# Kernel tuning notes

Measured on AMD Instinct MI355X. Metric: run time of the kernel, lower is better.

The kernel has to match this reference:

```python
import jax, jax.numpy as jnp
import numpy as np

B, S, D, K, DF, H, DFF = 2, 512, 512, 8, 64, 8, 2048
DH = D // H  # d_head = 64
CS = D // K  # chunk_size = 64


def layer_norm(x, g, b, eps=1e-5):
    m = x.mean(-1, keepdims=True)
    v = ((x - m) ** 2).mean(-1, keepdims=True)
    return (x - m) / jnp.sqrt(v + eps) * g + b


def matexp_taylor(M, terms=6):
    # exp(M) ~= I + M + M^2/2! + ... (6 terms), batched over leading dims
    I = jnp.broadcast_to(jnp.eye(M.shape[-1], dtype=M.dtype), M.shape)
    res, P = I, I
    for n in range(1, terms + 1):
        P = jnp.matmul(P, M) / n
        res = res + P
    return res


def setup_inputs() -> dict:
    key = jax.random.key(0)
    ks = jax.random.split(key, 24)
    w = lambda k, shape, s=0.02: (jax.random.normal(k, shape, jnp.float32) * s)
    return {
        'x': jax.random.normal(ks[0], (B, S, D), jnp.float32),
        'u': jax.random.normal(ks[1], (B, S, DF), jnp.float32),
        'Wq': w(ks[2], (D, D)), 'bq': jnp.zeros((D,), jnp.float32),
        'Wk': w(ks[3], (D, D)), 'bk': jnp.zeros((D,), jnp.float32),
        'Wv': w(ks[4], (D, D)), 'bv': jnp.zeros((D,), jnp.float32),
        'Wo': w(ks[5], (D, D)), 'bo': jnp.zeros((D,), jnp.float32),
        'Wfp': w(ks[6], (DF, D)), 'bfp': jnp.zeros((D,), jnp.float32),
        'Wfo': w(ks[7], (D, DF)), 'bfo': jnp.zeros((DF,), jnp.float32),
        'Wc1': w(ks[8], (D, DFF)), 'bc1': jnp.zeros((DFF,), jnp.float32),
        'g_ln': jnp.ones((DFF,), jnp.float32), 'b_ln': jnp.zeros((DFF,), jnp.float32),
        # small scale keeps the Lie elements O(1) so the Taylor matexp is well-behaved
        'Wc2': w(ks[9], (DFF, D * K * K), 0.001), 'bc2': jnp.zeros((D * K * K,), jnp.float32),
    }


def reference(x, u, Wq, bq, Wk, bk, Wv, bv, Wo, bo, Wfp, bfp, Wfo, bfo,
              Wc1, bc1, g_ln, b_ln, Wc2, bc2):
    b, s, d = x.shape
    # --- ConnectionNetwork: A[b,s,d,k,k] ---
    h = jax.nn.gelu(x @ Wc1 + bc1, approximate=False)
    h = layer_norm(h, g_ln, b_ln)
    A = (h @ Wc2 + bc2).reshape(b, s, d, K, K)
    # --- ParallelTransport: lie[b,i,j] = sum_d (x_i - x_j)_d * A[j,d]  ---
    # (split into x_i.A_j and x_j.A_j terms to avoid [b,s,s,d,k,k] intermediate)
    lie = jnp.einsum('bid,bjdkl->bijkl', x, A) - jnp.einsum('bjd,bjdkl->bjkl', x, A)[:, None]
    Gamma = matexp_taylor(-lie)  # [b,s,s,k,k], Gamma[b,i,j] transports j->i
    # --- standard multi-head attention on x (eval mode, no dropout, no mask) ---
    q = (x @ Wq + bq).reshape(b, s, H, DH).transpose(0, 2, 1, 3)
    k_ = (x @ Wk + bk).reshape(b, s, H, DH).transpose(0, 2, 1, 3)
    v = (x @ Wv + bv).reshape(b, s, H, DH).transpose(0, 2, 1, 3)
    scores = jnp.einsum('bhid,bhjd->bhij', q, k_) / jnp.sqrt(jnp.float32(DH))
    attn = jax.nn.softmax(scores, axis=-1)
    ctx = jnp.einsum('bhij,bhjd->bhid', attn, v).transpose(0, 2, 1, 3).reshape(b, s, d)
    x_out = x + ctx @ Wo + bo
    # --- fiber transport: u_i += sum_j attn_avg[i,j] * Gamma[i,j] @ u_chunks[j] ---
    u_proj = u @ Wfp + bfp                      # [b,s,D]
    u_chunks = u_proj.reshape(b, s, K, CS)      # [b,s,k,cs]
    attn_avg = attn.mean(axis=1)                # [b,s,s]
    weighted = Gamma * attn_avg[..., None, None]
    u_t = jnp.einsum('bijkl,bjlc->bikc', weighted, u_chunks).reshape(b, s, d)
    u_out = u + u_t @ Wfo + bfo
    return (x_out, u_out)
```

## Files before the change

kernel.cpp:

```cpp
#include <hip/hip_runtime.h>
#include <math.h>

#define BB 2
#define SS 512
#define DD 512
#define HH 8
#define DFF 2048

typedef __attribute__((ext_vector_type(8))) short bf16x8;
typedef __attribute__((ext_vector_type(4))) float f32x4;

__device__ __forceinline__ float gelu_exact(float v) {
    return 0.5f * v * (1.0f + erff(v * 0.70710678118654752f));
}
__device__ __forceinline__ unsigned short f2bf(float f) {
    unsigned u = __float_as_uint(f);
    u += 0x7FFF + ((u >> 16) & 1);
    return (unsigned short)(u >> 16);
}
__device__ __forceinline__ float bf2f(unsigned short s) {
    return __uint_as_float(((unsigned)s) << 16);
}
__device__ __forceinline__ void gload16(const void* g, void* l) {
    __builtin_amdgcn_global_load_lds((const __attribute__((address_space(1))) void*)g,
                                     (__attribute__((address_space(3))) void*)l, 16, 0, 0);
}

template<int NT, int EPI>
__global__ __launch_bounds__(256)
void mgemm_k(const unsigned short* __restrict__ A, const unsigned short* __restrict__ B,
             const float* __restrict__ bias, const float* __restrict__ resid,
             float* __restrict__ Cf, unsigned short* __restrict__ Cb,
             int K, int lda, int ldb, int ldc, int batchH,
             long aSB, long aSH, long bSB, long bSH, long cSB, long cSH,
             float scale)
{
    __shared__ unsigned short As[128][32];
    __shared__ unsigned short Bs[NT][32];
    const int tid = threadIdx.x;
    const int wave = tid >> 6, lane = tid & 63;
    const int z = blockIdx.z;
    const int zb = z / batchH, zh = z % batchH;
    const unsigned short* Ab = A + (long)zb * aSB + (long)zh * aSH;
    const unsigned short* Bb = B + (long)zb * bSB + (long)zh * bSH;
    const int row0 = blockIdx.y * 128, col0 = blockIdx.x * NT;
    const int wm = wave >> 1, wn = wave & 1;
    const int lm = lane & 15, quad = lane >> 4;
    const int lrow = lane >> 2, lk = (lane & 3) * 8;
    constexpr int NTW = NT / 32;
    f32x4 acc[4][NTW];
    #pragma unroll
    for (int i = 0; i < 4; ++i)
        #pragma unroll
        for (int j = 0; j < NTW; ++j) acc[i][j] = (f32x4)0.f;

    for (int k0 = 0; k0 < K; k0 += 32) {
        #pragma unroll
        for (int t = 0; t < 2; ++t) {
            const int r = wave * 32 + t * 16;
            gload16(Ab + (long)(row0 + r + lrow) * lda + k0 + lk, &As[r][0]);
        }
        if (NT == 128) {
            #pragma unroll
            for (int t = 0; t < 2; ++t) {
                const int r = wave * 32 + t * 16;
                gload16(Bb + (long)(col0 + r + lrow) * ldb + k0 + lk, &Bs[r][0]);
            }
        } else {
            const int r = wave * 16;
            gload16(Bb + (long)(col0 + r + lrow) * ldb + k0 + lk, &Bs[r][0]);
        }
        __syncthreads();
        bf16x8 af[4], bfr[NTW];
        #pragma unroll
        for (int mt = 0; mt < 4; ++mt)
            af[mt] = *(const bf16x8*)&As[wm * 64 + mt * 16 + lm][quad * 8];
        #pragma unroll
        for (int nt = 0; nt < NTW; ++nt)
            bfr[nt] = *(const bf16x8*)&Bs[wn * (NT / 2) + nt * 16 + lm][quad * 8];
        #pragma unroll
        for (int mt = 0; mt < 4; ++mt)
            #pragma unroll
            for (int nt = 0; nt < NTW; ++nt)
                acc[mt][nt] = __builtin_amdgcn_mfma_f32_16x16x32_bf16(
                    af[mt], bfr[nt], acc[mt][nt], 0, 0, 0);
        __syncthreads();
    }
    float* Cfz = Cf ? Cf + (long)zb * cSB + (long)zh * cSH : nullptr;
    unsigned short* Cbz = Cb ? Cb + (long)zb * cSB + (long)zh * cSH : nullptr;
    #pragma unroll
    for (int mt = 0; mt < 4; ++mt) {
        #pragma unroll
        for (int nt = 0; nt < NTW; ++nt) {
            #pragma unroll
            for (int r = 0; r < 4; ++r) {
                const int row = row0 + wm * 64 + mt * 16 + quad * 4 + r;
                const int col = col0 + wn * (NT / 2) + nt * 16 + lm;
                float v = acc[mt][nt][r] * scale;
                if (EPI == 2)      v += bias[(col & 511) * 64 + (col >> 9)];
                else if (EPI == 1 || EPI == 4) v += bias[col];
                else if ((EPI == 3 || EPI == 5 || EPI == 6) && bias) v += bias[col];
                if (EPI == 1) v = gelu_exact(v);
                if (EPI == 4) v += resid[(long)row * ldc + col];
                if (EPI == 0 || EPI == 1 || EPI == 4)
                    Cfz[(long)row * ldc + col] = v;
                else if (EPI == 2 || EPI == 3)
                    Cbz[(long)row * ldc + col] = f2bf(v);
                else if (EPI == 5)
                    Cb[(long)(row >> 9) * 262144 + (col >> 6) * 32768 +
                       (col & 63) * 512 + (row & 511)] = f2bf(v);
                else if (EPI == 6)
                    Cb[(long)(row >> 9) * 262144 + (col & 63) * 4096 +
                       (row & 511) * 8 + (col >> 6)] = f2bf(v);
            }
        }
    }
}

__global__ __launch_bounds__(512, 2)
void fc2_k(const unsigned short* __restrict__ A, const unsigned short* __restrict__ Bm,
           const float* __restrict__ bias, unsigned short* __restrict__ C)
{
    extern __shared__ unsigned short smraw[];
#define SMA(ab, h) (smraw + (((ab) * 2 + (h)) * 8192))
#define SMB(bb, h) (smraw + (32768 + ((bb) * 2 + (h)) * 8192))
    const int tid = threadIdx.x;
    const int wave = tid >> 6, lane = tid & 63;
    const int bid = blockIdx.x;
    const int lin = (bid & 7) * 64 + (bid >> 3);
    const int by = lin & 3, bx = lin >> 2;
    const int row0 = by * 256, col0 = bx * 256;
    const int wm = wave >> 2, wn = wave & 3;
    const int lm = lane & 15, quad = lane >> 4;
    const int axor = lm & 7;
    const int arow = (wm * 64 + lm) * 64;
    const int brow = (wn * 32 + lm) * 64;
    const int ca0 = ((quad) ^ axor) * 8;
    const int ca1 = ((quad + 4) ^ axor) * 8;
    const int srow = wave * 8 + (lane >> 3);
    const int scx = ((lane & 7) ^ ((lane >> 3) & 7)) * 8;
    const int sbrow = ((srow >> 5) << 6) + (srow & 31);
    const unsigned short* AgB = A + (long)(row0 + srow) * 2048 + scx;
    const unsigned short* BgB = Bm + (long)(col0 + sbrow) * 2048 + scx;

    f32x4 acc[8][4];
    #pragma unroll
    for (int i = 0; i < 8; ++i)
        #pragma unroll
        for (int j = 0; j < 4; ++j) acc[i][j] = (f32x4)0.f;
    bf16x8 afr[4][2], b0f[2][2], b1f[2][2];

#define STGA(ab, h, toff) do { \
        const unsigned short* _g = AgB + (toff) * 64 + (h) * (64 * 2048); \
        unsigned short* _d = SMA(ab, h) + wave * 512; \
        gload16(_g, _d); \
        gload16(_g + 128 * 2048, _d + 4096); \
    } while (0)
#define STGB(bb, h, toff) do { \
        const unsigned short* _g = BgB + (toff) * 64 + (h) * (32 * 2048); \
        unsigned short* _d = SMB(bb, h) + wave * 512; \
        gload16(_g, _d); \
        gload16(_g + 128 * 2048, _d + 4096); \
    } while (0)
#define RDA(Hp) do { _Pragma("unroll") for (int _m = 0; _m < 4; ++_m) { \
        afr[_m][0] = *(const bf16x8*)((Hp) + arow + _m * 1024 + ca0); \
        afr[_m][1] = *(const bf16x8*)((Hp) + arow + _m * 1024 + ca1); } } while (0)
#define RDB(bf, Hp) do { _Pragma("unroll") for (int _n = 0; _n < 2; ++_n) { \
        bf[_n][0] = *(const bf16x8*)((Hp) + brow + _n * 1024 + ca0); \
        bf[_n][1] = *(const bf16x8*)((Hp) + brow + _n * 1024 + ca1); } } while (0)
#define MM(QM, QN, bf) do { _Pragma("unroll") for (int _m = 0; _m < 4; ++_m) \
        _Pragma("unroll") for (int _n = 0; _n < 2; ++_n) { \
        acc[(QM)*4+_m][(QN)*2+_n] = __builtin_amdgcn_mfma_f32_16x16x32_bf16( \
            afr[_m][0], bf[_n][0], acc[(QM)*4+_m][(QN)*2+_n], 0, 0, 0); \
        acc[(QM)*4+_m][(QN)*2+_n] = __builtin_amdgcn_mfma_f32_16x16x32_bf16( \
            afr[_m][1], bf[_n][1], acc[(QM)*4+_m][(QN)*2+_n], 0, 0, 0); } } while (0)
#define PH_MID() \
        __builtin_amdgcn_s_barrier(); \
        asm volatile("s_waitcnt lgkmcnt(0)" ::: "memory"); \
        __builtin_amdgcn_sched_barrier(0); \
        __builtin_amdgcn_s_setprio(1)
#define PH_END(VM) \
        __builtin_amdgcn_s_setprio(0); \
        __builtin_amdgcn_sched_barrier(0); \
        asm volatile("s_waitcnt vmcnt(" #VM ")" ::: "memory"); \
        __builtin_amdgcn_sched_barrier(0); \
        __builtin_amdgcn_s_barrier()
#define PH_END_NW() \
        __builtin_amdgcn_s_setprio(0); \
        __builtin_amdgcn_sched_barrier(0); \
        __builtin_amdgcn_s_barrier()

    STGB(0, 0, 0);
    STGB(0, 1, 0);
    STGA(0, 0, 0);
    STGA(0, 1, 0);
    STGB(1, 0, 1);
    STGB(1, 1, 1);
    asm volatile("s_waitcnt vmcnt(6)" ::: "memory");
    __builtin_amdgcn_s_barrier();

    int rA = 0;
    int rB = 0, mB = 1, wB = 2;
    #pragma unroll 1
    for (int t = 0; t < 32; ++t) {
        const int tA = (t + 1 < 32) ? (t + 1) : 31;
        const int tB = (t + 2 < 32) ? (t + 2) : 31;
        const unsigned short* A0p = SMA(rA, 0);
        const unsigned short* A1p = SMA(rA, 1);
        const unsigned short* B0p = SMB(rB, 0);
        const unsigned short* B1p = SMB(rB, 1);
        RDA(A0p); RDB(b0f, B0p);
        STGA(rA ^ 1, 0, tA);
        PH_MID(); MM(0, 0, b0f); PH_END_NW();
        RDB(b1f, B1p);
        STGA(rA ^ 1, 1, tA);
        PH_MID(); MM(0, 1, b1f); PH_END(8);
        RDA(A1p);
        STGB(wB, 0, tB);
        PH_MID(); MM(1, 1, b1f); PH_END_NW();
        STGB(wB, 1, tB);
        PH_MID(); MM(1, 0, b0f); PH_END(6);
        rA ^= 1;
        const int tmp = rB; rB = mB; mB = wB; wB = tmp;
    }
    asm volatile("s_waitcnt vmcnt(0)" ::: "memory");

    const int crow = row0 + wm * 128 + quad * 4;
    const int ccol0 = col0 + wn * 64 + lm;
    #pragma unroll
    for (int ms = 0; ms < 8; ++ms)
        #pragma unroll
        for (int ns = 0; ns < 4; ++ns) {
            const int col = ccol0 + ns * 16;
            const float bv = bias[(col & 511) * 64 + (col >> 9)];
            #pragma unroll
            for (int r = 0; r < 4; ++r) {
                const int row = crow + ms * 16 + r;
                C[(long)row * 32768 + col] = f2bf(acc[ms][ns][r] + bv);
            }
        }
#undef SMA
#undef SMB
#undef STGA
#undef STGB
#undef RDA
#undef RDB
#undef MM
#undef PH_MID
#undef PH_END
#undef PH_END_NW
}

__global__ __launch_bounds__(256)
void liegamma_k(const unsigned short* __restrict__ xb, const unsigned short* __restrict__ At,
                const float* __restrict__ xa, const float* __restrict__ aavg,
                unsigned short* __restrict__ Gw)
{
    __shared__ unsigned short Xs[128][32];
    __shared__ unsigned short Ts[64][32];
    __shared__ float Ml[128][68];
    const int tid = threadIdx.x;
    const int wave = tid >> 6, lane = tid & 63;
    const int b = blockIdx.z, j = blockIdx.y;
    const int i0 = blockIdx.x * 128;
    const int lm = lane & 15, quad = lane >> 4;
    const int lrow = lane >> 2, lk = (lane & 3) * 8;
    const unsigned short* Xb = xb + ((long)b * 512 + i0) * 512;
    const unsigned short* Tb = At + ((long)(b * 512 + j)) * 32768;
    f32x4 acc[2][4];
    #pragma unroll
    for (int i = 0; i < 2; ++i)
        #pragma unroll
        for (int n = 0; n < 4; ++n) acc[i][n] = (f32x4)0.f;

    for (int k0 = 0; k0 < 512; k0 += 32) {
        #pragma unroll
        for (int t = 0; t < 2; ++t) {
            const int r = wave * 32 + t * 16;
            gload16(Xb + (long)(r + lrow) * 512 + k0 + lk, &Xs[r][0]);
        }
        {
            const int r = wave * 16;
            gload16(Tb + (long)(r + lrow) * 512 + k0 + lk, &Ts[r][0]);
        }
        __syncthreads();
        bf16x8 af[2], bfr[4];
        #pragma unroll
        for (int mt = 0; mt < 2; ++mt)
            af[mt] = *(const bf16x8*)&Xs[wave * 32 + mt * 16 + lm][quad * 8];
        #pragma unroll
        for (int nt = 0; nt < 4; ++nt)
            bfr[nt] = *(const bf16x8*)&Ts[nt * 16 + lm][quad * 8];
        #pragma unroll
        for (int mt = 0; mt < 2; ++mt)
            #pragma unroll
            for (int nt = 0; nt < 4; ++nt)
                acc[mt][nt] = __builtin_amdgcn_mfma_f32_16x16x32_bf16(
                    af[mt], bfr[nt], acc[mt][nt], 0, 0, 0);
        __syncthreads();
    }
    const float* xar = xa + ((long)(b * 512 + j)) * 64;
    #pragma unroll
    for (int mt = 0; mt < 2; ++mt)
        #pragma unroll
        for (int nt = 0; nt < 4; ++nt) {
            const float xv = xar[nt * 16 + lm];
            #pragma unroll
            for (int r = 0; r < 4; ++r)
                Ml[wave * 32 + mt * 16 + quad * 4 + r][nt * 16 + lm] = xv - acc[mt][nt][r];
        }
    __syncthreads();
    const int r8 = tid & 7, mg = tid >> 3;
    #pragma unroll 1
    for (int pass = 0; pass < 4; ++pass) {
        const int mi = pass * 32 + mg;
        const f32x4* Mr = (const f32x4*)&Ml[mi][0];
        f32x4 Mreg[16];
        #pragma unroll
        for (int l = 0; l < 16; ++l) Mreg[l] = Mr[l];
        float P[8], res[8];
        #pragma unroll
        for (int c = 0; c < 8; ++c) { const float iv = (c == r8) ? 1.f : 0.f; P[c] = iv; res[c] = iv; }
        #pragma unroll
        for (int n = 1; n <= 6; ++n) {
            float tmp[8] = {0.f,0.f,0.f,0.f,0.f,0.f,0.f,0.f};
            const float invn = 1.f / (float)n;
            #pragma unroll
            for (int l = 0; l < 8; ++l) {
                const f32x4 m0 = Mreg[l * 2], m1 = Mreg[l * 2 + 1];
                const float pl = P[l];
                #pragma unroll
                for (int c = 0; c < 4; ++c) {
                    tmp[c]     = fmaf(pl, m0[c], tmp[c]);
                    tmp[4 + c] = fmaf(pl, m1[c], tmp[4 + c]);
                }
            }
            #pragma unroll
            for (int c = 0; c < 8; ++c) { P[c] = tmp[c] * invn; res[c] += P[c]; }
        }
        const float av = aavg[((long)b * 512 + i0 + mi) * 512 + j];
        bf16x8 o;
        #pragma unroll
        for (int c = 0; c < 8; ++c) o[c] = (short)f2bf(res[c] * av);
        *(bf16x8*)(Gw + ((long)(b * 8 + r8) * 512 + (i0 + mi)) * 4096 + (long)j * 8) = o;
    }
}

__global__ __launch_bounds__(256)
void lnbf_k(const float* __restrict__ h, const float* __restrict__ g,
            const float* __restrict__ b, unsigned short* __restrict__ out)
{
    const long row = blockIdx.x;
    const float* r = h + row * (long)DFF;
    const int tid = threadIdx.x;
    float vals[8];
    float s = 0.f, sq = 0.f;
    #pragma unroll
    for (int e = 0; e < 8; ++e) {
        const float v = r[tid + e * 256];
        vals[e] = v; s += v; sq += v * v;
    }
    __shared__ float rs[256], rq[256];
    rs[tid] = s; rq[tid] = sq; __syncthreads();
    for (int st = 128; st > 0; st >>= 1) {
        if (tid < st) { rs[tid] += rs[tid + st]; rq[tid] += rq[tid + st]; }
        __syncthreads();
    }
    const float mean = rs[0] * (1.f / DFF);
    const float var  = rq[0] * (1.f / DFF) - mean * mean;
    const float inv  = rsqrtf(var + 1e-5f);
    unsigned short* o = out + row * (long)DFF;
    #pragma unroll
    for (int e = 0; e < 8; ++e) {
        const int c = tid + e * 256;
        o[c] = f2bf((vals[e] - mean) * inv * g[c] + b[c]);
    }
}

__global__ __launch_bounds__(256)
void xa_k(const float* __restrict__ x, const unsigned short* __restrict__ At,
          float* __restrict__ xa)
{
    const int bj = blockIdx.x;
    const int tid = threadIdx.x;
    const int kl = tid >> 2, q = tid & 3;
    const unsigned short* Ar = At + (long)bj * 32768 + kl * 512 + q * 128;
    const float* xr = x + (long)bj * 512 + q * 128;
    float s = 0.f;
    #pragma unroll
    for (int d0 = 0; d0 < 128; d0 += 8) {
        const bf16x8 a = *(const bf16x8*)&Ar[d0];
        const f32x4 x0 = *(const f32x4*)&xr[d0];
        const f32x4 x1 = *(const f32x4*)&xr[d0 + 4];
        s = fmaf(x0[0], bf2f((unsigned short)a[0]), s);
        s = fmaf(x0[1], bf2f((unsigned short)a[1]), s);
        s = fmaf(x0[2], bf2f((unsigned short)a[2]), s);
        s = fmaf(x0[3], bf2f((unsigned short)a[3]), s);
        s = fmaf(x1[0], bf2f((unsigned short)a[4]), s);
        s = fmaf(x1[1], bf2f((unsigned short)a[5]), s);
        s = fmaf(x1[2], bf2f((unsigned short)a[6]), s);
        s = fmaf(x1[3], bf2f((unsigned short)a[7]), s);
    }
    __shared__ float red[64][5];
    red[kl][q] = s; __syncthreads();
    if (q == 0)
        xa[(long)bj * 64 + kl] = red[kl][0] + red[kl][1] + red[kl][2] + red[kl][3];
}

__global__ __launch_bounds__(256)
void softmax_k(float* __restrict__ p, unsigned short* __restrict__ pb)
{
    const long row = blockIdx.x;
    float* r = p + row * 512;
    const int tid = threadIdx.x;
    float v0 = r[tid], v1 = r[tid + 256];
    __shared__ float red[256];
    red[tid] = fmaxf(v0, v1); __syncthreads();
    for (int s = 128; s > 0; s >>= 1) {
        if (tid < s) red[tid] = fmaxf(red[tid], red[tid + s]);
        __syncthreads();
    }
    const float m = red[0]; __syncthreads();
    v0 = expf(v0 - m); v1 = expf(v1 - m);
    red[tid] = v0 + v1; __syncthreads();
    for (int s = 128; s > 0; s >>= 1) {
        if (tid < s) red[tid] += red[tid + s];
        __syncthreads();
    }
    const float inv = 1.f / red[0];
    const float a0 = v0 * inv, a1 = v1 * inv;
    r[tid] = a0; r[tid + 256] = a1;
    unsigned short* rb = pb + row * 512;
    rb[tid] = f2bf(a0); rb[tid + 256] = f2bf(a1);
}

__global__ __launch_bounds__(256)
void aavg_k(const float* __restrict__ attn, float* __restrict__ aavg)
{
    const long idx = (long)blockIdx.x * 256 + threadIdx.x;
    const int b = (int)(idx >> 18);
    const long rem = idx & 262143;
    float s = 0.f;
    #pragma unroll
    for (int h = 0; h < HH; ++h)
        s += attn[(long)b * 2097152 + (long)h * 262144 + rem];
    aavg[idx] = s * 0.125f;
}

__global__ __launch_bounds__(256)
void tconv_k(const float* __restrict__ in, unsigned short* __restrict__ out,
             int R, int C)
{
    __shared__ float Ls[64][65];
    const int c0 = blockIdx.x * 64, r0 = blockIdx.y * 64;
    const int tid = threadIdx.x;
    const int tc = tid & 63, tr = tid >> 6;
    #pragma unroll
    for (int p = 0; p < 16; ++p)
        Ls[tr + p * 4][tc] = in[(long)(r0 + tr + p * 4) * C + c0 + tc];
    __syncthreads();
    #pragma unroll
    for (int p = 0; p < 16; ++p)
        out[(long)(c0 + tr + p * 4) * R + r0 + tc] = f2bf(Ls[tc][tr + p * 4]);
}

__global__ __launch_bounds__(256)
void wc2p_k(const float* __restrict__ in, unsigned short* __restrict__ out)
{
    __shared__ float Ls[64][65];
    const int d0 = blockIdx.x;
    const long f0 = blockIdx.y * 64;
    const int tid = threadIdx.x;
    const int tc = tid & 63, tr = tid >> 6;
    #pragma unroll
    for (int p = 0; p < 16; ++p)
        Ls[tr + p * 4][tc] = in[(f0 + tr + p * 4) * 32768 + (long)d0 * 64 + tc];
    __syncthreads();
    #pragma unroll
    for (int p = 0; p < 16; ++p) {
        const int kl = tr + p * 4;
        out[((long)kl * 512 + d0) * 2048 + f0 + tc] = f2bf(Ls[tc][kl]);
    }
}

__global__ __launch_bounds__(256)
void f2bf_k(const float* __restrict__ in, unsigned short* __restrict__ out, int n)
{
    const int i = blockIdx.x * 256 + threadIdx.x;
    if (i < n) out[i] = f2bf(in[i]);
}

extern "C" void kernel_launch(void* const* d_in, const int* in_sizes, int n_in,
                              void* d_out, int out_size, void* d_ws, size_t ws_size,
                              hipStream_t stream) {
    const float* x   = (const float*)d_in[0];
    const float* u   = (const float*)d_in[1];
    const float* Wq  = (const float*)d_in[2];  const float* bq  = (const float*)d_in[3];
    const float* Wk  = (const float*)d_in[4];  const float* bk  = (const float*)d_in[5];
    const float* Wv  = (const float*)d_in[6];  const float* bv  = (const float*)d_in[7];
    const float* Wo  = (const float*)d_in[8];  const float* bo  = (const float*)d_in[9];
    const float* Wfp = (const float*)d_in[10]; const float* bfp = (const float*)d_in[11];
    const float* Wfo = (const float*)d_in[12]; const float* bfo = (const float*)d_in[13];
    const float* Wc1 = (const float*)d_in[14]; const float* bc1 = (const float*)d_in[15];
    const float* gln = (const float*)d_in[16]; const float* bln = (const float*)d_in[17];
    const float* Wc2 = (const float*)d_in[18]; const float* bc2 = (const float*)d_in[19];

    float* ws = (float*)d_ws;
    unsigned short* Wc2p = (unsigned short*)(ws);
    unsigned short* Gw   = (unsigned short*)(ws);
    unsigned short* At   = (unsigned short*)(ws + 33554432);
    float*          h    = ws + 50331648;
    unsigned short* h_bf = (unsigned short*)(ws + 52428800);
    unsigned short* x_bf = (unsigned short*)(ws + 53477376);
    unsigned short* u_bf = (unsigned short*)(ws + 53739520);
    unsigned short* Wc1t = (unsigned short*)(ws + 53772288);
    unsigned short* Wqt  = (unsigned short*)(ws + 54296576);
    unsigned short* Wkt  = (unsigned short*)(ws + 54427648);
    unsigned short* Wvt  = (unsigned short*)(ws + 54558720);
    unsigned short* Wot  = (unsigned short*)(ws + 54689792);
    unsigned short* Wfpt = (unsigned short*)(ws + 54820864);
    unsigned short* Wfot = (unsigned short*)(ws + 54837248);
    float*          xa   = ws + 54853632;
    unsigned short* q_bf = (unsigned short*)(ws + 54919168);
    unsigned short* k_bf = (unsigned short*)(ws + 55181312);
    unsigned short* vT   = (unsigned short*)(ws + 55443456);
    float*          sc   = ws + 55705600;
    unsigned short* at_bf= (unsigned short*)(ws + 59899904);
    float*          av   = ws + 61997056;
    unsigned short* ctx  = (unsigned short*)(ws + 62521344);
    unsigned short* upT2 = (unsigned short*)(ws + 62783488);
    unsigned short* ut_bf= (unsigned short*)(ws + 63045632);
    float* xout = (float*)d_out;
    float* uout = xout + 524288;

    const dim3 blk(256);

    hipFuncSetAttribute(reinterpret_cast<const void*>(fc2_k),
                        hipFuncAttributeMaxDynamicSharedMemorySize, 163840);

    tconv_k<<<dim3(32, 8), blk, 0, stream>>>(Wc1, Wc1t, 512, 2048);
    tconv_k<<<dim3(8, 8), blk, 0, stream>>>(Wq, Wqt, 512, 512);
    tconv_k<<<dim3(8, 8), blk, 0, stream>>>(Wk, Wkt, 512, 512);
    tconv_k<<<dim3(8, 8), blk, 0, stream>>>(Wv, Wvt, 512, 512);
    tconv_k<<<dim3(8, 8), blk, 0, stream>>>(Wo, Wot, 512, 512);
    tconv_k<<<dim3(8, 1), blk, 0, stream>>>(Wfp, Wfpt, 64, 512);
    tconv_k<<<dim3(1, 8), blk, 0, stream>>>(Wfo, Wfot, 512, 64);
    wc2p_k<<<dim3(512, 32), blk, 0, stream>>>(Wc2, Wc2p);
    f2bf_k<<<dim3(2048), blk, 0, stream>>>(x, x_bf, 524288);
    f2bf_k<<<dim3(256), blk, 0, stream>>>(u, u_bf, 65536);

    mgemm_k<128,3><<<dim3(4, 8, 1), blk, 0, stream>>>(
        x_bf, Wqt, bq, nullptr, nullptr, q_bf, 512, 512, 512, 512,
        1, 0,0,0,0,0,0, 1.0f);
    mgemm_k<128,3><<<dim3(4, 8, 1), blk, 0, stream>>>(
        x_bf, Wkt, bk, nullptr, nullptr, k_bf, 512, 512, 512, 512,
        1, 0,0,0,0,0,0, 1.0f);
    mgemm_k<128,5><<<dim3(4, 8, 1), blk, 0, stream>>>(
        x_bf, Wvt, bv, nullptr, nullptr, vT, 512, 512, 512, 512,
        1, 0,0,0,0,0,0, 1.0f);
    mgemm_k<128,0><<<dim3(4, 4, 16), blk, 0, stream>>>(
        q_bf, k_bf, nullptr, nullptr, sc, nullptr, 64, 512, 512, 512,
        8, 262144,64, 262144,64, 2097152,262144, 0.125f);
    softmax_k<<<dim3(BB * HH * SS), blk, 0, stream>>>(sc, at_bf);
    aavg_k<<<dim3(2048), blk, 0, stream>>>(sc, av);
    mgemm_k<64,3><<<dim3(1, 4, 16), blk, 0, stream>>>(
        at_bf, vT, nullptr, nullptr, nullptr, ctx, 512, 512, 512, 512,
        8, 2097152,262144, 262144,32768, 262144,64, 1.0f);
    mgemm_k<128,4><<<dim3(4, 8, 1), blk, 0, stream>>>(
        ctx, Wot, bo, x, xout, nullptr, 512, 512, 512, 512,
        1, 0,0,0,0,0,0, 1.0f);

    mgemm_k<128,1><<<dim3(16, 8, 1), blk, 0, stream>>>(
        x_bf, Wc1t, bc1, nullptr, h, nullptr, 512, 512, 512, 2048,
        1, 0,0,0,0,0,0, 1.0f);
    lnbf_k<<<dim3(1024), blk, 0, stream>>>(h, gln, bln, h_bf);
    fc2_k<<<dim3(512), dim3(512), 163840, stream>>>(h_bf, Wc2p, bc2, At);
    xa_k<<<dim3(1024), blk, 0, stream>>>(x, At, xa);
    liegamma_k<<<dim3(4, 512, 2), blk, 0, stream>>>(x_bf, At, xa, av, Gw);

    mgemm_k<128,6><<<dim3(4, 8, 1), blk, 0, stream>>>(
        u_bf, Wfpt, bfp, nullptr, nullptr, upT2, 64, 64, 64, 512,
        1, 0,0,0,0,0,0, 1.0f);
    mgemm_k<64,3><<<dim3(1, 4, 16), blk, 0, stream>>>(
        Gw, upT2, nullptr, nullptr, nullptr, ut_bf, 4096, 4096, 4096, 512,
        8, 16777216,2097152, 262144,0, 262144,64, 1.0f);
    mgemm_k<64,4><<<dim3(1, 8, 1), blk, 0, stream>>>(
        ut_bf, Wfot, bfo, u, uout, nullptr, 512, 512, 512, 64,
        1, 0,0,0,0,0,0, 1.0f);
}
```

Before: 944.1 us.

## Split-K the small GEMMs with separate fp32 partial-sum reduction kernels

Adds a split-K template parameter to the MFMA GEMM so each block covers only a slice of the K dimension and writes fp32 partials. The Q/K/V projections, attn@V, the Wo projection, the Gamma-weighted transport GEMM and the Wfo projection now launch 4-8x more blocks. Small reduction kernels then sum the partials and apply bias, residual and layout transforms. This targets low occupancy on a large-CU GPU, since those GEMMs previously launched only 16-64 blocks. The cost is extra kernel launches and extra global traffic for the fp32 partials.

Result: faster. 866.1 us (-8.3%).

```diff
diff --git a/kernel.cpp b/kernel.cpp
--- a/kernel.cpp
+++ b/kernel.cpp
@@ -26,7 +26,7 @@
                                      (__attribute__((address_space(3))) void*)l, 16, 0, 0);
 }
 
-template<int NT, int EPI>
+template<int NT, int EPI, int SK = 1>
 __global__ __launch_bounds__(256)
 void mgemm_k(const unsigned short* __restrict__ A, const unsigned short* __restrict__ B,
              const float* __restrict__ bias, const float* __restrict__ resid,
@@ -43,7 +43,9 @@
     const int zb = z / batchH, zh = z % batchH;
     const unsigned short* Ab = A + (long)zb * aSB + (long)zh * aSH;
     const unsigned short* Bb = B + (long)zb * bSB + (long)zh * bSH;
-    const int row0 = blockIdx.y * 128, col0 = blockIdx.x * NT;
+    const int chunk = (SK > 1) ? ((int)blockIdx.x % SK) : 0;
+    const int colb  = (SK > 1) ? ((int)blockIdx.x / SK) : (int)blockIdx.x;
+    const int row0 = blockIdx.y * 128, col0 = colb * NT;
     const int wm = wave >> 1, wn = wave & 1;
     const int lm = lane & 15, quad = lane >> 4;
     const int lrow = lane >> 2, lk = (lane & 3) * 8;
@@ -54,7 +56,8 @@
         #pragma unroll
         for (int j = 0; j < NTW; ++j) acc[i][j] = (f32x4)0.f;
 
-    for (int k0 = 0; k0 < K; k0 += 32) {
+    const int kLo = chunk * (K / SK), kHi = kLo + K / SK;
+    for (int k0 = kLo; k0 < kHi; k0 += 32) {
         #pragma unroll
         for (int t = 0; t < 2; ++t) {
             const int r = wave * 32 + t * 16;
@@ -86,7 +89,7 @@
                     af[mt], bfr[nt], acc[mt][nt], 0, 0, 0);
         __syncthreads();
     }
-    float* Cfz = Cf ? Cf + (long)zb * cSB + (long)zh * cSH : nullptr;
+    float* Cfz = (Cf && EPI != 7) ? Cf + (long)zb * cSB + (long)zh * cSH : Cf;
     unsigned short* Cbz = Cb ? Cb + (long)zb * cSB + (long)zh * cSH : nullptr;
     #pragma unroll
     for (int mt = 0; mt < 4; ++mt) {
@@ -104,6 +107,8 @@
                 if (EPI == 4) v += resid[(long)row * ldc + col];
                 if (EPI == 0 || EPI == 1 || EPI == 4)
                     Cfz[(long)row * ldc + col] = v;
+                else if (EPI == 7)
+                    Cf[(long)z * cSB + (long)chunk * cSH + (long)row * ldc + col] = v;
                 else if (EPI == 2 || EPI == 3)
                     Cbz[(long)row * ldc + col] = f2bf(v);
                 else if (EPI == 5)
@@ -115,6 +120,56 @@
             }
         }
     }
+}
+
+__global__ __launch_bounds__(256)
+void redqk_k(const float* __restrict__ p, const float* __restrict__ bias,
+             unsigned short* __restrict__ out)
+{
+    const long idx = (long)blockIdx.x * 256 + threadIdx.x;
+    const float s = p[idx] + p[idx + 524288] + p[idx + 1048576] + p[idx + 1572864]
+                  + bias[idx & 511];
+    out[idx] = f2bf(s);
+}
+__global__ __launch_bounds__(256)
+void redv_k(const float* __restrict__ p, const float* __restrict__ bias,
+            unsigned short* __restrict__ vT)
+{
+    const long idx = (long)blockIdx.x * 256 + threadIdx.x;
+    const int col = (int)(idx & 511);
+    const float s = p[idx] + p[idx + 524288] + p[idx + 1048576] + p[idx + 1572864]
+                  + bias[col];
+    vT[(idx >> 18) * 262144 + (col >> 6) * 32768 + (col & 63) * 512 +
+       ((idx >> 9) & 511)] = f2bf(s);
+}
+__global__ __launch_bounds__(256)
+void redwo_k(const float* __restrict__ p, const float* __restrict__ bias,
+             const float* __restrict__ resid, float* __restrict__ out)
+{
+    const long idx = (long)blockIdx.x * 256 + threadIdx.x;
+    out[idx] = resid[idx] + bias[idx & 511]
+             + p[idx] + p[idx + 524288] + p[idx + 1048576] + p[idx + 1572864];
+}
+template<int SK>
+__global__ __launch_bounds__(256)
+void redzc_k(const float* __restrict__ p, unsigned short* __restrict__ out)
+{
+    const long idx = (long)blockIdx.x * 256 + threadIdx.x;
+    float s = 0.f;
+    #pragma unroll
+    for (int k = 0; k < SK; ++k) s += p[idx + (long)k * 524288];
+    const int b = (int)(idx >> 18), zh = (int)((idx >> 15) & 7);
+    const long rem = idx & 32767;
+    const int i = (int)(rem >> 6), c = (int)(rem & 63);
+    out[(long)b * 262144 + (long)i * 512 + zh * 64 + c] = f2bf(s);
+}
+__global__ __launch_bounds__(256)
+void redu_k(const float* __restrict__ p, const float* __restrict__ bias,
+            const float* __restrict__ resid, float* __restrict__ out)
+{
+    const long idx = (long)blockIdx.x * 256 + threadIdx.x;
+    out[idx] = resid[idx] + bias[idx & 63]
+             + p[idx] + p[idx + 65536] + p[idx + 131072] + p[idx + 196608];
 }
 
 __global__ __launch_bounds__(512, 2)
@@ -530,6 +585,13 @@
     unsigned short* ctx  = (unsigned short*)(ws + 62521344);
     unsigned short* upT2 = (unsigned short*)(ws + 62783488);
     unsigned short* ut_bf= (unsigned short*)(ws + 63045632);
+    float*          qp   = ws + 63307776;
+    float*          kp   = ws + 65404928;
+    float*          vp   = ws + 67502080;
+    float*          wop  = ws + 69599232;
+    float*          ctxp = ws + 71696384;
+    float*          utp  = ws + 73793536;
+    float*          up   = ws + 77987840;
     float* xout = (float*)d_out;
     float* uout = xout + 524288;
 
@@ -549,26 +611,31 @@
     f2bf_k<<<dim3(2048), blk, 0, stream>>>(x, x_bf, 524288);
     f2bf_k<<<dim3(256), blk, 0, stream>>>(u, u_bf, 65536);
 
-    mgemm_k<128,3><<<dim3(4, 8, 1), blk, 0, stream>>>(
-        x_bf, Wqt, bq, nullptr, nullptr, q_bf, 512, 512, 512, 512,
-        1, 0,0,0,0,0,0, 1.0f);
-    mgemm_k<128,3><<<dim3(4, 8, 1), blk, 0, stream>>>(
-        x_bf, Wkt, bk, nullptr, nullptr, k_bf, 512, 512, 512, 512,
-        1, 0,0,0,0,0,0, 1.0f);
-    mgemm_k<128,5><<<dim3(4, 8, 1), blk, 0, stream>>>(
-        x_bf, Wvt, bv, nullptr, nullptr, vT, 512, 512, 512, 512,
-        1, 0,0,0,0,0,0, 1.0f);
+    mgemm_k<128,7,4><<<dim3(16, 8, 1), blk, 0, stream>>>(
+        x_bf, Wqt, nullptr, nullptr, qp, nullptr, 512, 512, 512, 512,
+        1, 0,0,0,0, 0,524288, 1.0f);
+    redqk_k<<<dim3(2048), blk, 0, stream>>>(qp, bq, q_bf);
+    mgemm_k<128,7,4><<<dim3(16, 8, 1), blk, 0, stream>>>(
+        x_bf, Wkt, nullptr, nullptr, kp, nullptr, 512, 512, 512, 512,
+        1, 0,0,0,0, 0,524288, 1.0f);
+    redqk_k<<<dim3(2048), blk, 0, stream>>>(kp, bk, k_bf);
+    mgemm_k<128,7,4><<<dim3(16, 8, 1), blk, 0, stream>>>(
+        x_bf, Wvt, nullptr, nullptr, vp, nullptr, 512, 512, 512, 512,
+        1, 0,0,0,0, 0,524288, 1.0f);
+    redv_k<<<dim3(2048), blk, 0, stream>>>(vp, bv, vT);
     mgemm_k<128,0><<<dim3(4, 4, 16), blk, 0, stream>>>(
         q_bf, k_bf, nullptr, nullptr, sc, nullptr, 64, 512, 512, 512,
         8, 262144,64, 262144,64, 2097152,262144, 0.125f);
     softmax_k<<<dim3(BB * HH * SS), blk, 0, stream>>>(sc, at_bf);
     aavg_k<<<dim3(2048), blk, 0, stream>>>(sc, av);
-    mgemm_k<64,3><<<dim3(1, 4, 16), blk, 0, stream>>>(
-        at_bf, vT, nullptr, nullptr, nullptr, ctx, 512, 512, 512, 512,
-        8, 2097152,262144, 262144,32768, 262144,64, 1.0f);
-    mgemm_k<128,4><<<dim3(4, 8, 1), blk, 0, stream>>>(
-        ctx, Wot, bo, x, xout, nullptr, 512, 512, 512, 512,
-        1, 0,0,0,0,0,0, 1.0f);
+    mgemm_k<64,7,4><<<dim3(4, 4, 16), blk, 0, stream>>>(
+        at_bf, vT, nullptr, nullptr, ctxp, nullptr, 512, 512, 512, 64,
+        8, 2097152,262144, 262144,32768, 32768,524288, 1.0f);
+    redzc_k<4><<<dim3(2048), blk, 0, stream>>>(ctxp, ctx);
+    mgemm_k<128,7,4><<<dim3(16, 8, 1), blk, 0, stream>>>(
+        ctx, Wot, nullptr, nullptr, wop, nullptr, 512, 512, 512, 512,
+        1, 0,0,0,0, 0,524288, 1.0f);
+    redwo_k<<<dim3(2048), blk, 0, stream>>>(wop, bo, x, xout);
 
     mgemm_k<128,1><<<dim3(16, 8, 1), blk, 0, stream>>>(
         x_bf, Wc1t, bc1, nullptr, h, nullptr, 512, 512, 512, 2048,
@@ -581,10 +648,12 @@
     mgemm_k<128,6><<<dim3(4, 8, 1), blk, 0, stream>>>(
         u_bf, Wfpt, bfp, nullptr, nullptr, upT2, 64, 64, 64, 512,
         1, 0,0,0,0,0,0, 1.0f);
-    mgemm_k<64,3><<<dim3(1, 4, 16), blk, 0, stream>>>(
-        Gw, upT2, nullptr, nullptr, nullptr, ut_bf, 4096, 4096, 4096, 512,
-        8, 16777216,2097152, 262144,0, 262144,64, 1.0f);
-    mgemm_k<64,4><<<dim3(1, 8, 1), blk, 0, stream>>>(
-        ut_bf, Wfot, bfo, u, uout, nullptr, 512, 512, 512, 64,
-        1, 0,0,0,0,0,0, 1.0f);
-}
+    mgemm_k<64,7,8><<<dim3(8, 4, 16), blk, 0, stream>>>(
+        Gw, upT2, nullptr, nullptr, utp, nullptr, 4096, 4096, 4096, 64,
+        8, 16777216,2097152, 262144,0, 32768,524288, 1.0f);
+    redzc_k<8><<<dim3(2048), blk, 0, stream>>>(utp, ut_bf);
+    mgemm_k<64,7,4><<<dim3(4, 8, 1), blk, 0, stream>>>(
+        ut_bf, Wfot, nullptr, nullptr, up, nullptr, 512, 512, 512, 64,
+        1, 0,0,0,0, 0,65536, 1.0f);
+    redu_k<<<dim3(256), blk, 0, stream>>>(up, bfo, u, uout);
+}
```
